# Kernel optimization log

Measured on AMD Instinct MI355X. Metric: run time of the kernel, lower is better.

Reference implementation:

```python
import jax, jax.numpy as jnp
import numpy as np

DIM, K, B, H, W = 256, 7, 16, 56, 56
EPS = 1e-5

def _conv(x, w, pad, groups=1):
    return jax.lax.conv_general_dilated(
        x, w, window_strides=(1, 1), padding=[(pad, pad), (pad, pad)],
        dimension_numbers=('NCHW', 'OIHW', 'NCHW'), feature_group_count=groups)

def _bn(x, g, b, m, v):
    scale = g / jnp.sqrt(v + EPS)          # [C]
    bias = b - m * scale
    return x * scale[None, :, None, None] + bias[None, :, None, None]

def _silu(x):
    return x * jax.nn.sigmoid(x)

def setup_inputs() -> dict:
    key = jax.random.key(0)
    ks = jax.random.split(key, 12)
    f = lambda k_, shp, s=0.05: jax.random.normal(k_, shp, jnp.float32) * s
    d = {
        'x':   jax.random.normal(ks[0], (B, DIM, H, W), jnp.float32),
        # RepConv branch: dense 3x3 conv + BN, dense 1x1 conv + BN
        'w3':  f(ks[1], (DIM, DIM, 3, 3)),
        'g1':  1.0 + f(ks[2], (DIM,)), 'b1': f(ks[3], (DIM,)),
        'm1':  f(ks[4], (DIM,)),       'v1': jax.random.uniform(ks[4], (DIM,), jnp.float32) + 0.5,
        'w1':  f(ks[5], (DIM, DIM, 1, 1)),
        'g2':  1.0 + f(ks[6], (DIM,)), 'b2': f(ks[7], (DIM,)),
        'm2':  f(ks[8], (DIM,)),       'v2': jax.random.uniform(ks[8], (DIM,), jnp.float32) + 0.5,
        # depthwise branches
        'dw7': f(ks[9], (DIM, 1, 7, 7)),
        'dwk': f(ks[10], (DIM, 1, K, K)),
        # final BN
        'g3':  1.0 + f(ks[11], (DIM,)), 'b3': f(ks[11], (DIM,)),
        'm3':  f(ks[11], (DIM,)),       'v3': jax.random.uniform(ks[11], (DIM,), jnp.float32) + 0.5,
    }
    return d

def reference(x, w3, g1, b1, m1, v1, w1, g2, b2, m2, v2, dw7, dwk, g3, b3, m3, v3):
    # RepConv (train-mode, bn=False): SiLU(BN(conv3x3(x)) + BN(conv1x1(x)))
    rep = _silu(_bn(_conv(x, w3, 1), g1, b1, m1, v1)
                + _bn(_conv(x, w1, 0), g2, b2, m2, v2))
    # parallel depthwise branches
    y = rep + _conv(x, dw7, 3, groups=DIM) + _conv(x, dwk, K // 2, groups=DIM)
    return _silu(_bn(y, g3, b3, m3, v3))
```

## Files before the change

kernel.cpp:

```cpp
#include <hip/hip_runtime.h>
#include <stdint.h>
#include <stddef.h>

#define DIM 256
#define NB 16
#define HH 56
#define WW 56
#define HWP (HH*WW)
#define PH 62
#define PW 62
#define NPIX (NB*HWP)
#define EPSV 1e-5f

using f32x4  = __attribute__((ext_vector_type(4))) float;
using bf16x8 = __attribute__((ext_vector_type(8))) __bf16;

static __device__ __forceinline__ unsigned short f2bf(float f) {
    union { float f; unsigned u; } v; v.f = f;
    unsigned r = v.u + 0x7FFFu + ((v.u >> 16) & 1u);
    return (unsigned short)(r >> 16);
}
static __device__ __forceinline__ float bf2f(unsigned short u) {
    union { unsigned u; float f; } v; v.u = ((unsigned)u) << 16; return v.f;
}
static __device__ __forceinline__ float silu_f(float z) {
    return z / (1.f + __expf(-z));
}

__global__ void prep_weights(
    const float* __restrict__ w3, const float* __restrict__ g1, const float* __restrict__ b1,
    const float* __restrict__ m1, const float* __restrict__ v1, const float* __restrict__ w1,
    const float* __restrict__ g2, const float* __restrict__ b2, const float* __restrict__ m2,
    const float* __restrict__ v2, const float* __restrict__ dw7, const float* __restrict__ dwk,
    const float* __restrict__ g3, const float* __restrict__ b3, const float* __restrict__ m3,
    const float* __restrict__ v3,
    unsigned short* __restrict__ WkT, float* __restrict__ dwm, float* __restrict__ biasm,
    float* __restrict__ sc3, float* __restrict__ bi3)
{
    int co = blockIdx.x, t = threadIdx.x;
    float s1 = g1[co] * rsqrtf(v1[co] + EPSV);
    float s2 = g2[co] * rsqrtf(v2[co] + EPSV);
    float w1v = w1[co*DIM + t] * s2;
    const float* w3r = w3 + (size_t)(co*DIM + t)*9;
#pragma unroll
    for (int s = 0; s < 9; ++s) {
        float v = w3r[s]*s1 + (s == 4 ? w1v : 0.f);
        WkT[((size_t)s*DIM + co)*DIM + t] = f2bf(v);
    }
    if (t < 49) dwm[co*49 + t] = dw7[co*49 + t] + dwk[co*49 + t];
    if (t == 0) {
        biasm[co] = (b1[co] - m1[co]*s1) + (b2[co] - m2[co]*s2);
        float s3 = g3[co] * rsqrtf(v3[co] + EPSV);
        sc3[co] = s3;
        bi3[co] = b3[co] - m3[co]*s3;
    }
}

__global__ void prep_xpad(const float* __restrict__ x, unsigned short* __restrict__ xpad)
{
    __shared__ float lds[64][57];
    int cc = blockIdx.x;
    int ph = blockIdx.y;
    int b  = blockIdx.z;
    int t  = threadIdx.x;
    int c0 = cc*64;
    char* rowc = (char*)xpad + ((size_t)(b*PH + ph)*PW)*(DIM*2) + c0*2;

    if (ph < 3 || ph >= HH + 3) {
        uint4 z = {0u,0u,0u,0u};
#pragma unroll
        for (int j = 0; j < 2; ++j) {
            int idx = j*256 + t;
            if (idx < 496) {
                int pix = idx >> 3, q = idx & 7;
                *(uint4*)(rowc + (size_t)pix*(DIM*2) + q*16) = z;
            }
        }
        return;
    }
    if (t < 48) {
        int p = t >> 3, q = t & 7;
        int pw = (p < 3) ? p : (PW - 6 + p);
        uint4 z = {0u,0u,0u,0u};
        *(uint4*)(rowc + (size_t)pw*(DIM*2) + q*16) = z;
    }
    int h = ph - 3;
#pragma unroll
    for (int j = 0; j < 14; ++j) {
        int idx = j*256 + t;
        int c = idx / 56, w = idx % 56;
        lds[c][w] = x[((size_t)(b*DIM + c0 + c)*HH + h)*WW + w];
    }
    __syncthreads();
#pragma unroll
    for (int j = 0; j < 7; ++j) {
        int idx = j*256 + t;
        int w = idx >> 5, cp = idx & 31;
        unsigned lo = f2bf(lds[2*cp][w]);
        unsigned hi = f2bf(lds[2*cp+1][w]);
        unsigned val = lo | (hi << 16);
        *(unsigned*)(rowc + (size_t)(w + 3)*(DIM*2) + 4*cp) = val;
    }
}

__global__ void depthwise7(const float* __restrict__ x, const float* __restrict__ dwm,
                           unsigned short* __restrict__ dwout)
{
    __shared__ float plane[PH][64];
    int c = blockIdx.x, b = blockIdx.y, t = threadIdx.x;
#pragma unroll
    for (int j = 0; j < 4; ++j) {
        int idx = j*256 + t;
        if (idx < 992) ((f32x4*)plane)[idx] = (f32x4){0.f,0.f,0.f,0.f};
    }
    __syncthreads();
    const float* xp = x + ((size_t)b*DIM + c)*HWP;
#pragma unroll
    for (int j = 0; j < 13; ++j) {
        int idx = j*256 + t;
        if (idx < HWP) {
            int h = idx / 56, w = idx % 56;
            plane[h + 3][w + 3] = xp[idx];
        }
    }
    float wr[49];
#pragma unroll
    for (int i = 0; i < 49; ++i) wr[i] = dwm[c*49 + i];
    __syncthreads();
    unsigned short* op = dwout + ((size_t)b*DIM + c)*HWP;
#pragma unroll
    for (int j = 0; j < 2; ++j) {
        int q = j*256 + t;
        if (q < 392) {
            int h = q / 7, w0 = (q % 7)*8;
            float a[8] = {0.f,0.f,0.f,0.f,0.f,0.f,0.f,0.f};
#pragma unroll
            for (int dy = 0; dy < 7; ++dy) {
                const float* row = &plane[h + dy][w0];
                union { f32x4 v[4]; float s[16]; } rr;
                rr.v[0] = *(const f32x4*)(row);
                rr.v[1] = *(const f32x4*)(row + 4);
                rr.v[2] = *(const f32x4*)(row + 8);
                rr.v[3] = *(const f32x4*)(row + 12);
#pragma unroll
                for (int dx = 0; dx < 7; ++dx) {
                    float wv = wr[dy*7 + dx];
#pragma unroll
                    for (int o = 0; o < 8; ++o) a[o] += rr.s[dx + o] * wv;
                }
            }
            uint4 pk;
            pk.x = (unsigned)f2bf(a[0]) | ((unsigned)f2bf(a[1]) << 16);
            pk.y = (unsigned)f2bf(a[2]) | ((unsigned)f2bf(a[3]) << 16);
            pk.z = (unsigned)f2bf(a[4]) | ((unsigned)f2bf(a[5]) << 16);
            pk.w = (unsigned)f2bf(a[6]) | ((unsigned)f2bf(a[7]) << 16);
            *(uint4*)&op[h*WW + w0] = pk;
        }
    }
}

__global__ __launch_bounds__(256, 2)
void main_conv(const unsigned short* __restrict__ xpad, const unsigned short* __restrict__ WkT,
               const unsigned short* __restrict__ dwo, const float* __restrict__ biasm,
               const float* __restrict__ sc3, const float* __restrict__ bi3,
               float* __restrict__ out)
{
    __shared__ __align__(16) char smem[65536];
    int t = threadIdx.x;
    int lane = t & 63, wv = t >> 6;
    int wm = wv >> 1, wn = wv & 1;
    int qm = lane & 15, qg = lane >> 4;

    int swz = (((lane & 7) ^ ((lane >> 3) & 7)) << 4);

    uintptr_t gA[4], gB[4];
#pragma unroll
    for (int r = 0; r < 4; ++r) {
        int pixt = r*32 + wv*8 + (lane >> 3);
        int P = blockIdx.x*128 + pixt;
        int bb = P / HWP, rem = P % HWP;
        int h = rem / WW, w = rem % WW;
        gA[r] = (uintptr_t)xpad + ((size_t)((bb*PH + h + 2)*PW + (w + 2))*DIM)*2 + swz;
        int cog = blockIdx.y*128 + pixt;
        gB[r] = (uintptr_t)WkT + ((size_t)cog*DIM)*2 + swz;
    }

    f32x4 acc[4][4] = {};

    auto stage = [&](int s, int buf) {
        int s9 = s >> 2, ch = s & 3;
        int ky = s9 / 3, kx = s9 - ky*3;
        int offA = (ky*PW + kx)*(DIM*2) + ch*128;
        int offB = s9*(DIM*DIM*2) + ch*128;
        char* base = smem + buf*32768;
#pragma unroll
        for (int r = 0; r < 4; ++r) {
            __builtin_amdgcn_global_load_lds(
                (const __attribute__((address_space(1))) void*)(gA[r] + offA),
                (__attribute__((address_space(3))) void*)(base + (r*32 + wv*8)*128),
                16, 0, 0);
            __builtin_amdgcn_global_load_lds(
                (const __attribute__((address_space(1))) void*)(gB[r] + offB),
                (__attribute__((address_space(3))) void*)(base + 16384 + (r*32 + wv*8)*128),
                16, 0, 0);
        }
    };

    int kxo = (qg << 4) ^ ((lane & 7) << 4);
    auto compute = [&](int buf) {
        const char* pA = smem + buf*32768 + (wm*64 + qm)*128;
        const char* pB = smem + buf*32768 + 16384 + (wn*64 + qm)*128;
#pragma unroll
        for (int kk = 0; kk < 2; ++kk) {
            int ko = kxo ^ (kk << 6);
            bf16x8 a[4], b[4];
#pragma unroll
            for (int i = 0; i < 4; ++i) {
                a[i] = *(const bf16x8*)(pA + i*2048 + ko);
                b[i] = *(const bf16x8*)(pB + i*2048 + ko);
            }
            __builtin_amdgcn_s_setprio(1);
#pragma unroll
            for (int i = 0; i < 4; ++i)
#pragma unroll
                for (int j = 0; j < 4; ++j)
                    acc[i][j] = __builtin_amdgcn_mfma_f32_16x16x32_bf16(a[i], b[j], acc[i][j], 0, 0, 0);
            __builtin_amdgcn_s_setprio(0);
        }
    };

#define VMW8() asm volatile("s_waitcnt vmcnt(8)" ::: "memory")
#define VMW0() asm volatile("s_waitcnt vmcnt(0)" ::: "memory")
#define BARX() { asm volatile("" ::: "memory"); __builtin_amdgcn_s_barrier(); asm volatile("" ::: "memory"); }

    stage(0, 0);
    stage(1, 1);
    VMW8(); BARX();
#pragma unroll 1
    for (int s = 0; s < 36; ++s) {
        compute(s & 1);
        BARX();
        if (s <= 33) {
            stage(s + 2, s & 1);
            VMW8();
            BARX();
        } else if (s == 34) {
            VMW0();
            BARX();
        }
    }
#undef VMW8
#undef VMW0
#undef BARX

    float* ep = (float*)smem + wv*1088;
#pragma unroll 1
    for (int mi = 0; mi < 4; ++mi) {
#pragma unroll
        for (int ni = 0; ni < 4; ++ni)
#pragma unroll
            for (int r = 0; r < 4; ++r)
                ep[(ni*16 + qm)*17 + 4*qg + r] = acc[mi][ni][r];
        int P = blockIdx.x*128 + wm*64 + mi*16 + qm;
        int bb = P / HWP, rem = P % HWP;
        size_t obase = (size_t)bb*DIM*HWP + rem;
#pragma unroll
        for (int j = 0; j < 16; ++j) {
            int col = j*4 + qg;
            int cog = blockIdx.y*128 + wn*64 + col;
            float z = ep[col*17 + qm] + biasm[cog];
            float rep = silu_f(z);
            float y = rep + bf2f(dwo[obase + (size_t)cog*HWP]);
            float yy = y * sc3[cog] + bi3[cog];
            out[obase + (size_t)cog*HWP] = silu_f(yy);
        }
    }
}

extern "C" void kernel_launch(void* const* d_in, const int* in_sizes, int n_in,
                              void* d_out, int out_size, void* d_ws, size_t ws_size,
                              hipStream_t stream)
{
    (void)in_sizes; (void)n_in; (void)out_size; (void)ws_size;
    const float* x   = (const float*)d_in[0];
    const float* w3  = (const float*)d_in[1];
    const float* g1  = (const float*)d_in[2];
    const float* b1  = (const float*)d_in[3];
    const float* m1  = (const float*)d_in[4];
    const float* v1  = (const float*)d_in[5];
    const float* w1  = (const float*)d_in[6];
    const float* g2  = (const float*)d_in[7];
    const float* b2  = (const float*)d_in[8];
    const float* m2  = (const float*)d_in[9];
    const float* v2  = (const float*)d_in[10];
    const float* dw7 = (const float*)d_in[11];
    const float* dwk = (const float*)d_in[12];
    const float* g3  = (const float*)d_in[13];
    const float* b3  = (const float*)d_in[14];
    const float* m3  = (const float*)d_in[15];
    const float* v3  = (const float*)d_in[16];
    float* out = (float*)d_out;

    char* ws = (char*)d_ws;
    unsigned short* xpad = (unsigned short*)(ws);
    unsigned short* WkT  = (unsigned short*)(ws + 31490048);
    unsigned short* dwo  = (unsigned short*)(ws + 32669696);
    float* dwm   = (float*)(ws + 58359808);
    float* biasm = (float*)(ws + 58409984);
    float* sc3   = (float*)(ws + 58411008);
    float* bi3   = (float*)(ws + 58412032);

    prep_weights<<<dim3(DIM), dim3(256), 0, stream>>>(
        w3, g1, b1, m1, v1, w1, g2, b2, m2, v2, dw7, dwk, g3, b3, m3, v3,
        WkT, dwm, biasm, sc3, bi3);
    prep_xpad<<<dim3(4, PH, NB), dim3(256), 0, stream>>>(x, xpad);
    depthwise7<<<dim3(DIM, NB), dim3(256), 0, stream>>>(x, dwm, dwo);
    main_conv<<<dim3(NPIX/128, 2), dim3(256), 0, stream>>>(xpad, WkT, dwo, biasm, sc3, bi3, out);
}
```

Before: 170.6 us.

## Switch main conv GEMM to 32x32x16 MFMA with matching epilogue layout

Replaces the 4x4 grid of 16x16x32 bf16 MFMAs per wave with a 2x2 grid of 32x32x16 MFMAs, changing the LDS fragment reads and swizzle offsets to match. This cuts the number of LDS fragment loads per K-step and uses the larger MFMA shape, which has higher throughput per instruction. The epilogue is rewritten to transpose 32-pixel tiles through a larger padded LDS region, and a barrier is added before it. The cost is a larger epilogue LDS footprint and explicit waitcnt/sched barriers, which may serialize some of the epilogue work.

```diff
diff --git a/kernel.cpp b/kernel.cpp
--- a/kernel.cpp
+++ b/kernel.cpp
@@ -13,6 +13,7 @@
 #define EPSV 1e-5f
 
 using f32x4  = __attribute__((ext_vector_type(4))) float;
+using f32x16 = __attribute__((ext_vector_type(16))) float;
 using bf16x8 = __attribute__((ext_vector_type(8))) __bf16;
 
 static __device__ __forceinline__ unsigned short f2bf(float f) {
@@ -169,7 +170,8 @@
     int t = threadIdx.x;
     int lane = t & 63, wv = t >> 6;
     int wm = wv >> 1, wn = wv & 1;
-    int qm = lane & 15, qg = lane >> 4;
+    int r5 = lane & 31, hi = lane >> 5, l7 = lane & 7;
+    int bx = blockIdx.x;
 
     int swz = (((lane & 7) ^ ((lane >> 3) & 7)) << 4);
 
@@ -177,7 +179,7 @@
 #pragma unroll
     for (int r = 0; r < 4; ++r) {
         int pixt = r*32 + wv*8 + (lane >> 3);
-        int P = blockIdx.x*128 + pixt;
+        int P = bx*128 + pixt;
         int bb = P / HWP, rem = P % HWP;
         int h = rem / WW, w = rem % WW;
         gA[r] = (uintptr_t)xpad + ((size_t)((bb*PH + h + 2)*PW + (w + 2))*DIM)*2 + swz;
@@ -185,7 +187,8 @@
         gB[r] = (uintptr_t)WkT + ((size_t)cog*DIM)*2 + swz;
     }
 
-    f32x4 acc[4][4] = {};
+    f32x16 acc00 = {}, acc01 = {}, acc10 = {}, acc11 = {};
+    bf16x8 a0, a1, b0, b1;
 
     auto stage = [&](int s, int buf) {
         int s9 = s >> 2, ch = s & 3;
@@ -206,27 +209,32 @@
         }
     };
 
-    int kxo = (qg << 4) ^ ((lane & 7) << 4);
+    const int cb0 = (((0 + hi) ^ l7) << 4);
+    const int cb1 = (((2 + hi) ^ l7) << 4);
+    const int cb2 = (((4 + hi) ^ l7) << 4);
+    const int cb3 = (((6 + hi) ^ l7) << 4);
+    const int rowb = r5 * 128;
+
+#define MFMA32 __builtin_amdgcn_mfma_f32_32x32x16_bf16
+#define KSTEP(pA, pB, cb) { \
+    a0 = *(const bf16x8*)((pA) + (cb)); \
+    a1 = *(const bf16x8*)((pA) + 4096 + (cb)); \
+    b0 = *(const bf16x8*)((pB) + (cb)); \
+    b1 = *(const bf16x8*)((pB) + 4096 + (cb)); \
+    __builtin_amdgcn_s_setprio(1); \
+    acc00 = MFMA32(a0, b0, acc00, 0, 0, 0); \
+    acc01 = MFMA32(a0, b1, acc01, 0, 0, 0); \
+    acc10 = MFMA32(a1, b0, acc10, 0, 0, 0); \
+    acc11 = MFMA32(a1, b1, acc11, 0, 0, 0); \
+    __builtin_amdgcn_s_setprio(0); }
+
     auto compute = [&](int buf) {
-        const char* pA = smem + buf*32768 + (wm*64 + qm)*128;
-        const char* pB = smem + buf*32768 + 16384 + (wn*64 + qm)*128;
-#pragma unroll
-        for (int kk = 0; kk < 2; ++kk) {
-            int ko = kxo ^ (kk << 6);
-            bf16x8 a[4], b[4];
-#pragma unroll
-            for (int i = 0; i < 4; ++i) {
-                a[i] = *(const bf16x8*)(pA + i*2048 + ko);
-                b[i] = *(const bf16x8*)(pB + i*2048 + ko);
-            }
-            __builtin_amdgcn_s_setprio(1);
-#pragma unroll
-            for (int i = 0; i < 4; ++i)
-#pragma unroll
-                for (int j = 0; j < 4; ++j)
-                    acc[i][j] = __builtin_amdgcn_mfma_f32_16x16x32_bf16(a[i], b[j], acc[i][j], 0, 0, 0);
-            __builtin_amdgcn_s_setprio(0);
-        }
+        const char* pA = smem + buf*32768 + wm*8192 + rowb;
+        const char* pB = smem + buf*32768 + 16384 + wn*8192 + rowb;
+        KSTEP(pA, pB, cb0)
+        KSTEP(pA, pB, cb1)
+        KSTEP(pA, pB, cb2)
+        KSTEP(pA, pB, cb3)
     };
 
 #define VMW8() asm volatile("s_waitcnt vmcnt(8)" ::: "memory")
@@ -251,30 +259,41 @@
     }
 #undef VMW8
 #undef VMW0
+
+    BARX();
 #undef BARX
 
-    float* ep = (float*)smem + wv*1088;
-#pragma unroll 1
-    for (int mi = 0; mi < 4; ++mi) {
-#pragma unroll
-        for (int ni = 0; ni < 4; ++ni)
-#pragma unroll
-            for (int r = 0; r < 4; ++r)
-                ep[(ni*16 + qm)*17 + 4*qg + r] = acc[mi][ni][r];
-        int P = blockIdx.x*128 + wm*64 + mi*16 + qm;
-        int bb = P / HWP, rem = P % HWP;
-        size_t obase = (size_t)bb*DIM*HWP + rem;
-#pragma unroll
-        for (int j = 0; j < 16; ++j) {
-            int col = j*4 + qg;
-            int cog = blockIdx.y*128 + wn*64 + col;
-            float z = ep[col*17 + qm] + biasm[cog];
-            float rep = silu_f(z);
-            float y = rep + bf2f(dwo[obase + (size_t)cog*HWP]);
-            float yy = y * sc3[cog] + bi3[cog];
-            out[obase + (size_t)cog*HWP] = silu_f(yy);
-        }
-    }
+    float* ep = (float*)smem + wv*2112;
+#define EPI(ti, aT0, aT1) { \
+    _Pragma("unroll") \
+    for (int rg = 0; rg < 16; ++rg) { \
+        int prow = (rg & 3) + 8*(rg >> 2) + 4*hi; \
+        ep[r5*33 + prow]        = aT0[rg]; \
+        ep[(32 + r5)*33 + prow] = aT1[rg]; \
+    } \
+    asm volatile("s_waitcnt lgkmcnt(0)" ::: "memory"); \
+    __builtin_amdgcn_sched_barrier(0); \
+    int P0 = bx*128 + wm*64 + (ti)*32;                  \
+    int bb = P0 / HWP, rem = P0 % HWP;                  \
+    size_t obase = (size_t)bb*DIM*HWP + rem + r5; \
+    _Pragma("unroll") \
+    for (int j2 = 0; j2 < 32; ++j2) { \
+        int cl = j2*2 + hi;                             \
+        int cog = blockIdx.y*128 + wn*64 + cl; \
+        float z = ep[cl*33 + r5] + biasm[cog]; \
+        float rep = silu_f(z); \
+        float y = rep + bf2f(dwo[obase + (size_t)cog*HWP]); \
+        float yy = y * sc3[cog] + bi3[cog]; \
+        out[obase + (size_t)cog*HWP] = silu_f(yy); \
+    } \
+    asm volatile("s_waitcnt lgkmcnt(0)" ::: "memory"); \
+    __builtin_amdgcn_sched_barrier(0); }
+
+    EPI(0, acc00, acc01)
+    EPI(1, acc10, acc11)
+#undef EPI
+#undef KSTEP
+#undef MFMA32
 }
 
 extern "C" void kernel_launch(void* const* d_in, const int* in_sizes, int n_in,
```

New measurement: 166.1 us. 1.03x faster.

## Halve K-tile to 32 channels to fit four blocks per CU

Applied to the files above, without the earlier changes.

The main implicit-GEMM conv now stages 32 input channels per K-step instead of 64. This halves shared memory to 32 KB double-buffered, and launch bounds rise to allow four blocks per CU. The load mapping, XOR swizzle and fragment offsets are rebuilt for 64-byte rows, and the loop runs 72 steps with adjusted waitcnt thresholds. The aim is higher occupancy to hide load latency, at the cost of twice as many barriers per output tile and a tighter register budget. The epilogue is also unrolled, with explicit LDS waits and scheduling barriers.

```diff
diff --git a/kernel.cpp b/kernel.cpp
--- a/kernel.cpp
+++ b/kernel.cpp
@@ -159,109 +159,109 @@
     }
 }
 
-__global__ __launch_bounds__(256, 2)
+__global__ __launch_bounds__(256, 4)
 void main_conv(const unsigned short* __restrict__ xpad, const unsigned short* __restrict__ WkT,
                const unsigned short* __restrict__ dwo, const float* __restrict__ biasm,
                const float* __restrict__ sc3, const float* __restrict__ bi3,
                float* __restrict__ out)
 {
-    __shared__ __align__(16) char smem[65536];
+    __shared__ __align__(16) char smem[32768];
     int t = threadIdx.x;
     int lane = t & 63, wv = t >> 6;
     int wm = wv >> 1, wn = wv & 1;
     int qm = lane & 15, qg = lane >> 4;
-
-    int swz = (((lane & 7) ^ ((lane >> 3) & 7)) << 4);
-
-    uintptr_t gA[4], gB[4];
-#pragma unroll
-    for (int r = 0; r < 4; ++r) {
-        int pixt = r*32 + wv*8 + (lane >> 3);
-        int P = blockIdx.x*128 + pixt;
+    int bx = blockIdx.x;
+
+    int swz = (((t & 3) ^ ((t >> 2) & 3)) << 4);
+
+    uintptr_t gA[2], gB[2];
+#pragma unroll
+    for (int p = 0; p < 2; ++p) {
+        int row = p*64 + (t >> 2);
+        int P = bx*128 + row;
         int bb = P / HWP, rem = P % HWP;
         int h = rem / WW, w = rem % WW;
-        gA[r] = (uintptr_t)xpad + ((size_t)((bb*PH + h + 2)*PW + (w + 2))*DIM)*2 + swz;
-        int cog = blockIdx.y*128 + pixt;
-        gB[r] = (uintptr_t)WkT + ((size_t)cog*DIM)*2 + swz;
+        gA[p] = (uintptr_t)xpad + ((size_t)((bb*PH + h + 2)*PW + (w + 2))*DIM)*2 + swz;
+        int cog = blockIdx.y*128 + row;
+        gB[p] = (uintptr_t)WkT + ((size_t)cog*DIM)*2 + swz;
     }
 
     f32x4 acc[4][4] = {};
 
-    auto stage = [&](int s, int buf) {
-        int s9 = s >> 2, ch = s & 3;
-        int ky = s9 / 3, kx = s9 - ky*3;
-        int offA = (ky*PW + kx)*(DIM*2) + ch*128;
-        int offB = s9*(DIM*DIM*2) + ch*128;
-        char* base = smem + buf*32768;
-#pragma unroll
-        for (int r = 0; r < 4; ++r) {
+    auto stage = [&](int kt, int buf) {
+        int tap = kt >> 3, cb = kt & 7;
+        int ky = tap / 3, kx = tap - ky*3;
+        int offA = (ky*PW + kx)*(DIM*2) + cb*64;
+        int offB = tap*(DIM*DIM*2) + cb*64;
+        char* base = smem + buf*16384;
+#pragma unroll
+        for (int p = 0; p < 2; ++p)
             __builtin_amdgcn_global_load_lds(
-                (const __attribute__((address_space(1))) void*)(gA[r] + offA),
-                (__attribute__((address_space(3))) void*)(base + (r*32 + wv*8)*128),
+                (const __attribute__((address_space(1))) void*)(gA[p] + offA),
+                (__attribute__((address_space(3))) void*)(base + p*4096 + t*16),
                 16, 0, 0);
+#pragma unroll
+        for (int p = 0; p < 2; ++p)
             __builtin_amdgcn_global_load_lds(
-                (const __attribute__((address_space(1))) void*)(gB[r] + offB),
-                (__attribute__((address_space(3))) void*)(base + 16384 + (r*32 + wv*8)*128),
+                (const __attribute__((address_space(1))) void*)(gB[p] + offB),
+                (__attribute__((address_space(3))) void*)(base + 8192 + p*4096 + t*16),
                 16, 0, 0);
-        }
     };
 
-    int kxo = (qg << 4) ^ ((lane & 7) << 4);
+    int ko = ((qg ^ (qm & 3)) << 4);
     auto compute = [&](int buf) {
-        const char* pA = smem + buf*32768 + (wm*64 + qm)*128;
-        const char* pB = smem + buf*32768 + 16384 + (wn*64 + qm)*128;
-#pragma unroll
-        for (int kk = 0; kk < 2; ++kk) {
-            int ko = kxo ^ (kk << 6);
-            bf16x8 a[4], b[4];
-#pragma unroll
-            for (int i = 0; i < 4; ++i) {
-                a[i] = *(const bf16x8*)(pA + i*2048 + ko);
-                b[i] = *(const bf16x8*)(pB + i*2048 + ko);
-            }
-            __builtin_amdgcn_s_setprio(1);
-#pragma unroll
-            for (int i = 0; i < 4; ++i)
-#pragma unroll
-                for (int j = 0; j < 4; ++j)
-                    acc[i][j] = __builtin_amdgcn_mfma_f32_16x16x32_bf16(a[i], b[j], acc[i][j], 0, 0, 0);
-            __builtin_amdgcn_s_setprio(0);
-        }
+        const char* pA = smem + buf*16384 + (wm*64 + qm)*64 + ko;
+        const char* pB = smem + buf*16384 + 8192 + (wn*64 + qm)*64 + ko;
+        bf16x8 a[4], b[4];
+#pragma unroll
+        for (int i = 0; i < 4; ++i) {
+            a[i] = *(const bf16x8*)(pA + i*1024);
+            b[i] = *(const bf16x8*)(pB + i*1024);
+        }
+        __builtin_amdgcn_s_setprio(1);
+#pragma unroll
+        for (int i = 0; i < 4; ++i)
+#pragma unroll
+            for (int j = 0; j < 4; ++j)
+                acc[i][j] = __builtin_amdgcn_mfma_f32_16x16x32_bf16(a[i], b[j], acc[i][j], 0, 0, 0);
+        __builtin_amdgcn_s_setprio(0);
     };
 
-#define VMW8() asm volatile("s_waitcnt vmcnt(8)" ::: "memory")
+#define VMW4() asm volatile("s_waitcnt vmcnt(4)" ::: "memory")
 #define VMW0() asm volatile("s_waitcnt vmcnt(0)" ::: "memory")
 #define BARX() { asm volatile("" ::: "memory"); __builtin_amdgcn_s_barrier(); asm volatile("" ::: "memory"); }
 
     stage(0, 0);
     stage(1, 1);
-    VMW8(); BARX();
+    VMW4(); BARX();
 #pragma unroll 1
-    for (int s = 0; s < 36; ++s) {
+    for (int s = 0; s < 72; ++s) {
         compute(s & 1);
         BARX();
-        if (s <= 33) {
+        if (s <= 69) {
             stage(s + 2, s & 1);
-            VMW8();
+            VMW4();
             BARX();
-        } else if (s == 34) {
+        } else if (s == 70) {
             VMW0();
             BARX();
         }
     }
-#undef VMW8
+#undef VMW4
 #undef VMW0
 #undef BARX
 
     float* ep = (float*)smem + wv*1088;
-#pragma unroll 1
+#pragma unroll
     for (int mi = 0; mi < 4; ++mi) {
 #pragma unroll
         for (int ni = 0; ni < 4; ++ni)
 #pragma unroll
             for (int r = 0; r < 4; ++r)
                 ep[(ni*16 + qm)*17 + 4*qg + r] = acc[mi][ni][r];
-        int P = blockIdx.x*128 + wm*64 + mi*16 + qm;
+        asm volatile("s_waitcnt lgkmcnt(0)" ::: "memory");
+        __builtin_amdgcn_sched_barrier(0);
+        int P = bx*128 + wm*64 + mi*16 + qm;
         int bb = P / HWP, rem = P % HWP;
         size_t obase = (size_t)bb*DIM*HWP + rem;
 #pragma unroll
@@ -274,6 +274,8 @@
             float yy = y * sc3[cog] + bi3[cog];
             out[obase + (size_t)cog*HWP] = silu_f(yy);
         }
+        asm volatile("s_waitcnt lgkmcnt(0)" ::: "memory");
+        __builtin_amdgcn_sched_barrier(0);
     }
 }
 
```

After: 178.9 us. 1.05x slower.

## Restructure main conv pipeline, swap grid order, reorder K loop channel-major

Applied to the files above, without the earlier changes.

Swaps the launch grid so the two output-channel blocks for the same pixel tile are adjacent. The intent is for them to share input tiles in L2. The K loop now walks channel chunks outer and taps inner. The hand-tuned double buffer (two stages in flight, explicit vmcnt waits, raw barriers and setprio) is replaced by an unrolled two-buffer loop that uses plain __syncthreads. The epilogue loop is also unrolled, with extra barriers added. The simpler synchronisation may drain all outstanding loads every half-step, which can reduce how much load latency is hidden behind MFMA work.

```diff
diff --git a/kernel.cpp b/kernel.cpp
--- a/kernel.cpp
+++ b/kernel.cpp
@@ -170,6 +170,8 @@
     int lane = t & 63, wv = t >> 6;
     int wm = wv >> 1, wn = wv & 1;
     int qm = lane & 15, qg = lane >> 4;
+    int bx = blockIdx.y;
+    int byc = blockIdx.x;
 
     int swz = (((lane & 7) ^ ((lane >> 3) & 7)) << 4);
 
@@ -177,21 +179,21 @@
 #pragma unroll
     for (int r = 0; r < 4; ++r) {
         int pixt = r*32 + wv*8 + (lane >> 3);
-        int P = blockIdx.x*128 + pixt;
+        int P = bx*128 + pixt;
         int bb = P / HWP, rem = P % HWP;
         int h = rem / WW, w = rem % WW;
         gA[r] = (uintptr_t)xpad + ((size_t)((bb*PH + h + 2)*PW + (w + 2))*DIM)*2 + swz;
-        int cog = blockIdx.y*128 + pixt;
+        int cog = byc*128 + pixt;
         gB[r] = (uintptr_t)WkT + ((size_t)cog*DIM)*2 + swz;
     }
 
     f32x4 acc[4][4] = {};
 
     auto stage = [&](int s, int buf) {
-        int s9 = s >> 2, ch = s & 3;
-        int ky = s9 / 3, kx = s9 - ky*3;
+        int ch = s / 9, tap = s - ch*9;
+        int ky = tap / 3, kx = tap - ky*3;
         int offA = (ky*PW + kx)*(DIM*2) + ch*128;
-        int offB = s9*(DIM*DIM*2) + ch*128;
+        int offB = tap*(DIM*DIM*2) + ch*128;
         char* base = smem + buf*32768;
 #pragma unroll
         for (int r = 0; r < 4; ++r) {
@@ -219,61 +221,49 @@
                 a[i] = *(const bf16x8*)(pA + i*2048 + ko);
                 b[i] = *(const bf16x8*)(pB + i*2048 + ko);
             }
-            __builtin_amdgcn_s_setprio(1);
 #pragma unroll
             for (int i = 0; i < 4; ++i)
 #pragma unroll
                 for (int j = 0; j < 4; ++j)
                     acc[i][j] = __builtin_amdgcn_mfma_f32_16x16x32_bf16(a[i], b[j], acc[i][j], 0, 0, 0);
-            __builtin_amdgcn_s_setprio(0);
         }
     };
 
-#define VMW8() asm volatile("s_waitcnt vmcnt(8)" ::: "memory")
-#define VMW0() asm volatile("s_waitcnt vmcnt(0)" ::: "memory")
-#define BARX() { asm volatile("" ::: "memory"); __builtin_amdgcn_s_barrier(); asm volatile("" ::: "memory"); }
-
     stage(0, 0);
-    stage(1, 1);
-    VMW8(); BARX();
+    __syncthreads();
 #pragma unroll 1
-    for (int s = 0; s < 36; ++s) {
-        compute(s & 1);
-        BARX();
-        if (s <= 33) {
-            stage(s + 2, s & 1);
-            VMW8();
-            BARX();
-        } else if (s == 34) {
-            VMW0();
-            BARX();
-        }
-    }
-#undef VMW8
-#undef VMW0
-#undef BARX
+    for (int it = 0; it < 18; ++it) {
+        stage(2*it + 1, 1);
+        compute(0);
+        __syncthreads();
+        if (it < 17) stage(2*it + 2, 0);
+        compute(1);
+        __syncthreads();
+    }
 
     float* ep = (float*)smem + wv*1088;
-#pragma unroll 1
+#pragma unroll
     for (int mi = 0; mi < 4; ++mi) {
 #pragma unroll
         for (int ni = 0; ni < 4; ++ni)
 #pragma unroll
             for (int r = 0; r < 4; ++r)
                 ep[(ni*16 + qm)*17 + 4*qg + r] = acc[mi][ni][r];
-        int P = blockIdx.x*128 + wm*64 + mi*16 + qm;
+        __syncthreads();
+        int P = bx*128 + wm*64 + mi*16 + qm;
         int bb = P / HWP, rem = P % HWP;
         size_t obase = (size_t)bb*DIM*HWP + rem;
 #pragma unroll
         for (int j = 0; j < 16; ++j) {
             int col = j*4 + qg;
-            int cog = blockIdx.y*128 + wn*64 + col;
+            int cog = byc*128 + wn*64 + col;
             float z = ep[col*17 + qm] + biasm[cog];
             float rep = silu_f(z);
             float y = rep + bf2f(dwo[obase + (size_t)cog*HWP]);
             float yy = y * sc3[cog] + bi3[cog];
             out[obase + (size_t)cog*HWP] = silu_f(yy);
         }
+        __syncthreads();
     }
 }
 
@@ -315,5 +305,5 @@
         WkT, dwm, biasm, sc3, bi3);
     prep_xpad<<<dim3(4, PH, NB), dim3(256), 0, stream>>>(x, xpad);
     depthwise7<<<dim3(DIM, NB), dim3(256), 0, stream>>>(x, dwm, dwo);
-    main_conv<<<dim3(NPIX/128, 2), dim3(256), 0, stream>>>(xpad, WkT, dwo, biasm, sc3, bi3, out);
-}
+    main_conv<<<dim3(2, NPIX/128), dim3(256), 0, stream>>>(xpad, WkT, dwo, biasm, sc3, bi3, out);
+}
```

New measurement: 146.5 us. -14.1%, faster.
